# Kernel optimization log

Measured on AMD Instinct MI355X. Metric: run time of the kernel, lower is better.

Reference implementation:

```python
import jax, jax.numpy as jnp
import numpy as np

INPUT_DIM = 1024
OUTPUT_DIM = 1024
DEGREE = 8


def setup_inputs() -> dict:
    key = jax.random.key(0)
    k1, k2 = jax.random.split(key)
    x = jax.random.normal(k1, (8192, INPUT_DIM), dtype=jnp.float32)
    std = 1.0 / (INPUT_DIM * (DEGREE + 1))
    cheby_coeffs = std * jax.random.normal(k2, (INPUT_DIM, OUTPUT_DIM, DEGREE + 1), dtype=jnp.float32)
    return {"x": x, "cheby_coeffs": cheby_coeffs}


def reference(x, cheby_coeffs):
    # x: (B, I); cheby_coeffs: (I, O, D+1)
    degree = cheby_coeffs.shape[-1] - 1
    xt = jnp.tanh(x.reshape(-1, cheby_coeffs.shape[0]))
    # Chebyshev recurrence T_0=1, T_1=x, T_k = 2*x*T_{k-1} - T_{k-2}
    polys = [jnp.ones_like(xt)]
    if degree > 0:
        polys.append(xt)
    for _ in range(2, degree + 1):
        polys.append(2.0 * xt * polys[-1] - polys[-2])
    cheby = jnp.stack(polys, axis=-1)  # (B, I, D+1)
    y = jnp.einsum('bid,iod->bo', cheby, cheby_coeffs)
    return y
```

## Files before the change

### kernel.cpp

```cpp
#include <hip/hip_runtime.h>
#include <hip/hip_bf16.h>

#define AS1 __attribute__((address_space(1)))
#define AS3 __attribute__((address_space(3)))

typedef __attribute__((ext_vector_type(8))) short bf16x8;
typedef __attribute__((ext_vector_type(4))) float f32x4;

#define KTOT 9216
#define NOUT 1024

__device__ __forceinline__ void gll16(const void* g, void* l) {
    __builtin_amdgcn_global_load_lds((const AS1 void*)g, (AS3 void*)l, 16, 0, 0);
}

__device__ __forceinline__ unsigned short f2bf(float f) {
    union { __hip_bfloat16 h; unsigned short u; } cv;
    cv.h = __float2bfloat16(f);
    return cv.u;
}

__device__ __forceinline__ float fast_tanhf(float v) {
    float e = __expf(2.0f * v);
    return 1.0f - 2.0f / (e + 1.0f);
}

__global__ void __launch_bounds__(256) prep_kernel(const float* __restrict__ cc,
                                                   unsigned short* __restrict__ Wt) {
    __shared__ unsigned short T[288 * 68];
    const int t  = threadIdx.x;
    const int n0 = (blockIdx.x & 31) * 32;
    const int i0 = (blockIdx.x >> 5) * 64;

    for (int il = 0; il < 64; ++il) {
        const float* src = cc + (size_t)(i0 + il) * KTOT + (size_t)n0 * 9;
        for (int f = t; f < 288; f += 256)
            T[f * 68 + il] = f2bf(src[f]);
    }
    __syncthreads();

    for (int it = 0; it < 18; ++it) {
        const int chunk = it * 16 + (t >> 4);
        const int nl = chunk / 9;
        const int d  = chunk - nl * 9;
        const int n  = n0 + nl;
        const int e0 = (t & 15) * 4;
        const int isrc = e0 ^ ((n & 7) << 3);
        ushort4 v = *(const ushort4*)&T[chunk * 68 + isrc];
        *(ushort4*)(Wt + (size_t)n * KTOT + d * 1024 + i0 + e0) = v;
    }
}

__global__ void __launch_bounds__(256, 2)
cheby_gemm(const float* __restrict__ x, const unsigned short* __restrict__ Wt,
           float* __restrict__ out) {
    __shared__ unsigned short Asub[128 * 64];
    __shared__ unsigned short Bsub[128 * 64];

    const int id   = blockIdx.x;
    const int bcol = (id & 7) * 128;
    const int brow = (id >> 3) * 128;
    const int t    = threadIdx.x;
    const int lane = t & 63;
    const int w    = t >> 6;
    const int wr   = (w >> 1) * 64;
    const int wc   = (w & 1) * 64;
    const int l15  = lane & 15;
    const int lhi  = lane >> 4;

    const int gi0 = (t & 15) * 4;
    const int gr  = t >> 4;

    const int bn_loc = t >> 3;
    const int bpos   = (t & 7) * 8;

    f32x4 acc[4][4] = {};

    float x2[8][4], Tp[8][4], Tpp[8][4];

    unsigned awoff[8];
#pragma unroll
    for (int p = 0; p < 8; ++p) {
        const int r = gr + 16 * p;
        awoff[p] = r * 128 + ((gi0 * 2) ^ ((r & 7) << 4));
    }

    for (int ic = 0; ic < 16; ++ic) {
#pragma unroll
        for (int p = 0; p < 8; ++p) {
            const float4 v = *(const float4*)(x + (size_t)(brow + gr + 16 * p) * 1024
                                              + ic * 64 + gi0);
            x2[p][0] = 2.0f * fast_tanhf(v.x);
            x2[p][1] = 2.0f * fast_tanhf(v.y);
            x2[p][2] = 2.0f * fast_tanhf(v.z);
            x2[p][3] = 2.0f * fast_tanhf(v.w);
        }
#pragma unroll
        for (int d = 0; d < 9; ++d) {
            __syncthreads();

            const int kb = d * 1024 + ic * 64;
#pragma unroll
            for (int c = 0; c < 4; ++c) {
                const unsigned short* src =
                    Wt + (size_t)(bcol + c * 32 + bn_loc) * KTOT + kb + bpos;
                gll16(src, (char*)Bsub + c * 4096 + w * 1024);
            }

#pragma unroll
            for (int p = 0; p < 8; ++p) {
                ushort4 pk;
                unsigned short* pks = (unsigned short*)&pk;
#pragma unroll
                for (int j = 0; j < 4; ++j) {
                    float cur;
                    if (d == 0) {
                        cur = 1.0f;
                    } else if (d == 1) {
                        cur = 0.5f * x2[p][j];
                        Tp[p][j] = cur;
                        Tpp[p][j] = 1.0f;
                    } else {
                        cur = __builtin_fmaf(x2[p][j], Tp[p][j], -Tpp[p][j]);
                        Tpp[p][j] = Tp[p][j];
                        Tp[p][j] = cur;
                    }
                    pks[j] = f2bf(cur);
                }
                *(ushort4*)((char*)Asub + awoff[p]) = pk;
            }

            __syncthreads();

#pragma unroll
            for (int ks = 0; ks < 2; ++ks) {
                bf16x8 af[4], bfr[4];
#pragma unroll
                for (int mf = 0; mf < 4; ++mf) {
                    const int row = wr + mf * 16 + l15;
                    af[mf] = *(const bf16x8*)((const char*)Asub + row * 128 +
                              ((ks * 64 + lhi * 16) ^ ((row & 7) << 4)));
                }
#pragma unroll
                for (int nf = 0; nf < 4; ++nf) {
                    const int n = wc + nf * 16 + l15;
                    bfr[nf] = *(const bf16x8*)((const char*)Bsub + n * 128 +
                              ((ks * 64 + lhi * 16) ^ ((n & 7) << 4)));
                }
#pragma unroll
                for (int mf = 0; mf < 4; ++mf)
#pragma unroll
                    for (int nf = 0; nf < 4; ++nf)
                        acc[mf][nf] = __builtin_amdgcn_mfma_f32_16x16x32_bf16(
                            af[mf], bfr[nf], acc[mf][nf], 0, 0, 0);
            }
        }
    }

#pragma unroll
    for (int mf = 0; mf < 4; ++mf)
#pragma unroll
        for (int nf = 0; nf < 4; ++nf)
#pragma unroll
            for (int ri = 0; ri < 4; ++ri) {
                const int orow = brow + wr + mf * 16 + lhi * 4 + ri;
                const int ocol = bcol + wc + nf * 16 + l15;
                out[(size_t)orow * NOUT + ocol] = acc[mf][nf][ri];
            }
}

__global__ void __launch_bounds__(256) naive_kernel(const float* __restrict__ x,
                                                    const float* __restrict__ cc,
                                                    float* __restrict__ out) {
    __shared__ float xs[1024];
    const int b = blockIdx.x;
    const int t = threadIdx.x;
#pragma unroll
    for (int j = 0; j < 4; ++j)
        xs[t * 4 + j] = fast_tanhf(x[(size_t)b * 1024 + t * 4 + j]);
    __syncthreads();

    const int o = t * 4;
    float a0 = 0.f, a1 = 0.f, a2 = 0.f, a3 = 0.f;
    for (int i = 0; i < 1024; ++i) {
        const float* cp = cc + (size_t)i * KTOT + (size_t)o * 9;
        const float xv = xs[i];
        float tpp = 1.0f, tp = xv;
        a0 += cp[0];  a1 += cp[9];  a2 += cp[18];  a3 += cp[27];
        a0 += xv * cp[1]; a1 += xv * cp[10]; a2 += xv * cp[19]; a3 += xv * cp[28];
#pragma unroll
        for (int d = 2; d <= 8; ++d) {
            const float cur = 2.0f * xv * tp - tpp;
            tpp = tp; tp = cur;
            a0 += cur * cp[d];      a1 += cur * cp[9 + d];
            a2 += cur * cp[18 + d]; a3 += cur * cp[27 + d];
        }
    }
    float* op = out + (size_t)b * NOUT + o;
    op[0] = a0; op[1] = a1; op[2] = a2; op[3] = a3;
}

extern "C" void kernel_launch(void* const* d_in, const int* in_sizes, int n_in,
                              void* d_out, int out_size, void* d_ws, size_t ws_size,
                              hipStream_t stream) {
    const float* x  = (const float*)d_in[0];
    const float* cc = (const float*)d_in[1];
    float* out = (float*)d_out;

    const size_t need = (size_t)KTOT * 1024 * sizeof(unsigned short);
    if (ws_size >= need) {
        prep_kernel<<<512, 256, 0, stream>>>(cc, (unsigned short*)d_ws);
        cheby_gemm<<<512, 256, 0, stream>>>(x, (const unsigned short*)d_ws, out);
    } else {
        naive_kernel<<<8192, 256, 0, stream>>>(x, cc, out);
    }
}
```

Before: 232.3 us.

## Fold T0 term into bias, load B fragments from global with double-buffered A tile

Removes the degree-0 Chebyshev term from the GEMM: because T0=1, its contribution is a per-output bias (sum of coefficients over inputs), which prep_kernel computes with atomics and the epilogue adds. This shrinks K from 9216 to 8192. The GEMM tile becomes 64x256 with each wave reading B fragments straight from global into registers, prefetched one step ahead. A is double-buffered in LDS so each step needs only one barrier. In exchange it adds a memset and atomics, and direct global B loads may be less coalesced than the previous LDS staging.

Result: slower. 312.7 us (+34.6%).

```diff
diff --git a/kernel.cpp b/kernel.cpp
--- a/kernel.cpp
+++ b/kernel.cpp
@@ -1,171 +1,202 @@
 #include <hip/hip_runtime.h>
 #include <hip/hip_bf16.h>
 
-#define AS1 __attribute__((address_space(1)))
-#define AS3 __attribute__((address_space(3)))
-
 typedef __attribute__((ext_vector_type(8))) short bf16x8;
 typedef __attribute__((ext_vector_type(4))) float f32x4;
 
-#define KTOT 9216
+#define CSTRIDE 9216
+#define KT2 8192
 #define NOUT 1024
 
-__device__ __forceinline__ void gll16(const void* g, void* l) {
-    __builtin_amdgcn_global_load_lds((const AS1 void*)g, (AS3 void*)l, 16, 0, 0);
-}
-
-__device__ __forceinline__ unsigned short f2bf(float f) {
+static __device__ __forceinline__ unsigned short f2bf(float f) {
     union { __hip_bfloat16 h; unsigned short u; } cv;
     cv.h = __float2bfloat16(f);
     return cv.u;
 }
-
-__device__ __forceinline__ float fast_tanhf(float v) {
+static __device__ __forceinline__ float bf2f(unsigned short u) {
+    union { float f; unsigned v; } c; c.v = (unsigned)u << 16; return c.f;
+}
+static __device__ __forceinline__ float fast_tanhf(float v) {
     float e = __expf(2.0f * v);
     return 1.0f - 2.0f / (e + 1.0f);
 }
 
 __global__ void __launch_bounds__(256) prep_kernel(const float* __restrict__ cc,
-                                                   unsigned short* __restrict__ Wt) {
+                                                   unsigned short* __restrict__ Wt,
+                                                   float* __restrict__ bias) {
     __shared__ unsigned short T[288 * 68];
     const int t  = threadIdx.x;
     const int n0 = (blockIdx.x & 31) * 32;
     const int i0 = (blockIdx.x >> 5) * 64;
 
     for (int il = 0; il < 64; ++il) {
-        const float* src = cc + (size_t)(i0 + il) * KTOT + (size_t)n0 * 9;
+        const float* src = cc + (size_t)(i0 + il) * CSTRIDE + (size_t)n0 * 9;
         for (int f = t; f < 288; f += 256)
             T[f * 68 + il] = f2bf(src[f]);
     }
     __syncthreads();
 
-    for (int it = 0; it < 18; ++it) {
+#pragma unroll
+    for (int it = 0; it < 16; ++it) {
         const int chunk = it * 16 + (t >> 4);
-        const int nl = chunk / 9;
-        const int d  = chunk - nl * 9;
-        const int n  = n0 + nl;
+        const int nl = chunk >> 3;
+        const int d  = (chunk & 7) + 1;
         const int e0 = (t & 15) * 4;
-        const int isrc = e0 ^ ((n & 7) << 3);
-        ushort4 v = *(const ushort4*)&T[chunk * 68 + isrc];
-        *(ushort4*)(Wt + (size_t)n * KTOT + d * 1024 + i0 + e0) = v;
+        ushort4 v = *(const ushort4*)&T[(nl * 9 + d) * 68 + e0];
+        *(ushort4*)(Wt + (size_t)(n0 + nl) * KT2 + (d - 1) * 1024 + i0 + e0) = v;
+    }
+
+    if (t < 32) {
+        float s = 0.f;
+#pragma unroll 8
+        for (int il = 0; il < 64; ++il) s += bf2f(T[(t * 9) * 68 + il]);
+        atomicAdd(&bias[n0 + t], s);
     }
 }
 
 __global__ void __launch_bounds__(256, 2)
 cheby_gemm(const float* __restrict__ x, const unsigned short* __restrict__ Wt,
-           float* __restrict__ out) {
-    __shared__ unsigned short Asub[128 * 64];
-    __shared__ unsigned short Bsub[128 * 64];
+           const float* __restrict__ bias, float* __restrict__ out) {
+    __shared__ unsigned short Asub[2][64 * 64];
 
     const int id   = blockIdx.x;
-    const int bcol = (id & 7) * 128;
-    const int brow = (id >> 3) * 128;
+    const int bcol = (id & 3) * 256;
+    const int brow = (id >> 2) * 64;
     const int t    = threadIdx.x;
     const int lane = t & 63;
     const int w    = t >> 6;
-    const int wr   = (w >> 1) * 64;
-    const int wc   = (w & 1) * 64;
+    const int wc   = w * 64;
     const int l15  = lane & 15;
     const int lhi  = lane >> 4;
 
     const int gi0 = (t & 15) * 4;
-    const int gr  = t >> 4;
-
-    const int bn_loc = t >> 3;
-    const int bpos   = (t & 7) * 8;
+    const int rr  = t >> 4;
+
+    unsigned awoff[4];
+#pragma unroll
+    for (int p = 0; p < 4; ++p) {
+        const int r = rr + 16 * p;
+        awoff[p] = r * 128 + ((gi0 * 2) ^ ((r & 7) << 4));
+    }
 
     f32x4 acc[4][4] = {};
-
-    float x2[8][4], Tp[8][4], Tpp[8][4];
-
-    unsigned awoff[8];
-#pragma unroll
-    for (int p = 0; p < 8; ++p) {
-        const int r = gr + 16 * p;
-        awoff[p] = r * 128 + ((gi0 * 2) ^ ((r & 7) << 4));
-    }
-
+    float x2[4][4], Tp[4][4], Tpp[4][4];
+    bf16x8 bcur[2][4];
+
+    const unsigned short* wbase = Wt + (size_t)(bcol + wc) * KT2 + lhi * 8;
+
+#pragma unroll
+    for (int p = 0; p < 4; ++p) {
+        const float4 v = *(const float4*)(x + (size_t)(brow + rr + 16 * p) * 1024 + gi0);
+        ushort4 pk; unsigned short* pks = (unsigned short*)&pk;
+#pragma unroll
+        for (int j = 0; j < 4; ++j) {
+            const float xv = (&v.x)[j];
+            x2[p][j] = 2.0f * fast_tanhf(xv);
+            const float c = 0.5f * x2[p][j];
+            Tp[p][j] = c; Tpp[p][j] = 1.0f;
+            pks[j] = f2bf(c);
+        }
+        *(ushort4*)((char*)Asub[0] + awoff[p]) = pk;
+    }
+#pragma unroll
+    for (int ks = 0; ks < 2; ++ks)
+#pragma unroll
+        for (int nf = 0; nf < 4; ++nf)
+            bcur[ks][nf] = *(const bf16x8*)(wbase + (size_t)(nf * 16 + l15) * KT2 + ks * 32);
+    asm volatile("s_waitcnt lgkmcnt(0)" ::: "memory");
+    __builtin_amdgcn_s_barrier();
+
+#pragma unroll 1
     for (int ic = 0; ic < 16; ++ic) {
 #pragma unroll
-        for (int p = 0; p < 8; ++p) {
-            const float4 v = *(const float4*)(x + (size_t)(brow + gr + 16 * p) * 1024
-                                              + ic * 64 + gi0);
-            x2[p][0] = 2.0f * fast_tanhf(v.x);
-            x2[p][1] = 2.0f * fast_tanhf(v.y);
-            x2[p][2] = 2.0f * fast_tanhf(v.z);
-            x2[p][3] = 2.0f * fast_tanhf(v.w);
-        }
-#pragma unroll
-        for (int d = 0; d < 9; ++d) {
-            __syncthreads();
-
-            const int kb = d * 1024 + ic * 64;
-#pragma unroll
-            for (int c = 0; c < 4; ++c) {
-                const unsigned short* src =
-                    Wt + (size_t)(bcol + c * 32 + bn_loc) * KTOT + kb + bpos;
-                gll16(src, (char*)Bsub + c * 4096 + w * 1024);
+        for (int dd = 0; dd < 8; ++dd) {
+            const int cur = dd & 1;
+            const int nxt = cur ^ 1;
+            const int ddn = (dd + 1) & 7;
+            const int icn = (dd == 7) ? ((ic + 1) & 15) : ic;
+            const int kbn = ddn * 1024 + icn * 64;
+
+            bf16x8 bnxt[2][4];
+#pragma unroll
+            for (int ks = 0; ks < 2; ++ks)
+#pragma unroll
+                for (int nf = 0; nf < 4; ++nf)
+                    bnxt[ks][nf] = *(const bf16x8*)(wbase + (size_t)(nf * 16 + l15) * KT2
+                                                    + kbn + ks * 32);
+
+            bf16x8 af[2][4];
+#pragma unroll
+            for (int ks = 0; ks < 2; ++ks)
+#pragma unroll
+                for (int mf = 0; mf < 4; ++mf) {
+                    const int row = mf * 16 + l15;
+                    af[ks][mf] = *(const bf16x8*)((const char*)Asub[cur] + row * 128 +
+                                  ((ks * 64 + lhi * 16) ^ ((row & 7) << 4)));
+                }
+
+            if (dd == 7) {
+#pragma unroll
+                for (int p = 0; p < 4; ++p) {
+                    const float4 v = *(const float4*)(x + (size_t)(brow + rr + 16 * p) * 1024
+                                                      + icn * 64 + gi0);
+                    ushort4 pk; unsigned short* pks = (unsigned short*)&pk;
+#pragma unroll
+                    for (int j = 0; j < 4; ++j) {
+                        const float xv = (&v.x)[j];
+                        x2[p][j] = 2.0f * fast_tanhf(xv);
+                        const float c = 0.5f * x2[p][j];
+                        Tp[p][j] = c; Tpp[p][j] = 1.0f;
+                        pks[j] = f2bf(c);
+                    }
+                    *(ushort4*)((char*)Asub[nxt] + awoff[p]) = pk;
+                }
+            } else {
+#pragma unroll
+                for (int p = 0; p < 4; ++p) {
+                    ushort4 pk; unsigned short* pks = (unsigned short*)&pk;
+#pragma unroll
+                    for (int j = 0; j < 4; ++j) {
+                        const float c = __builtin_fmaf(x2[p][j], Tp[p][j], -Tpp[p][j]);
+                        Tpp[p][j] = Tp[p][j]; Tp[p][j] = c;
+                        pks[j] = f2bf(c);
+                    }
+                    *(ushort4*)((char*)Asub[nxt] + awoff[p]) = pk;
+                }
             }
 
 #pragma unroll
-            for (int p = 0; p < 8; ++p) {
-                ushort4 pk;
-                unsigned short* pks = (unsigned short*)&pk;
-#pragma unroll
-                for (int j = 0; j < 4; ++j) {
-                    float cur;
-                    if (d == 0) {
-                        cur = 1.0f;
-                    } else if (d == 1) {
-                        cur = 0.5f * x2[p][j];
-                        Tp[p][j] = cur;
-                        Tpp[p][j] = 1.0f;
-                    } else {
-                        cur = __builtin_fmaf(x2[p][j], Tp[p][j], -Tpp[p][j]);
-                        Tpp[p][j] = Tp[p][j];
-                        Tp[p][j] = cur;
-                    }
-                    pks[j] = f2bf(cur);
-                }
-                *(ushort4*)((char*)Asub + awoff[p]) = pk;
-            }
-
-            __syncthreads();
-
-#pragma unroll
-            for (int ks = 0; ks < 2; ++ks) {
-                bf16x8 af[4], bfr[4];
-#pragma unroll
-                for (int mf = 0; mf < 4; ++mf) {
-                    const int row = wr + mf * 16 + l15;
-                    af[mf] = *(const bf16x8*)((const char*)Asub + row * 128 +
-                              ((ks * 64 + lhi * 16) ^ ((row & 7) << 4)));
-                }
-#pragma unroll
-                for (int nf = 0; nf < 4; ++nf) {
-                    const int n = wc + nf * 16 + l15;
-                    bfr[nf] = *(const bf16x8*)((const char*)Bsub + n * 128 +
-                              ((ks * 64 + lhi * 16) ^ ((n & 7) << 4)));
-                }
+            for (int ks = 0; ks < 2; ++ks)
 #pragma unroll
                 for (int mf = 0; mf < 4; ++mf)
 #pragma unroll
                     for (int nf = 0; nf < 4; ++nf)
                         acc[mf][nf] = __builtin_amdgcn_mfma_f32_16x16x32_bf16(
-                            af[mf], bfr[nf], acc[mf][nf], 0, 0, 0);
-            }
+                            af[ks][mf], bcur[ks][nf], acc[mf][nf], 0, 0, 0);
+
+            asm volatile("s_waitcnt lgkmcnt(0)" ::: "memory");
+            __builtin_amdgcn_s_barrier();
+
+#pragma unroll
+            for (int ks = 0; ks < 2; ++ks)
+#pragma unroll
+                for (int nf = 0; nf < 4; ++nf)
+                    bcur[ks][nf] = bnxt[ks][nf];
         }
     }
 
+    float bv[4];
+#pragma unroll
+    for (int nf = 0; nf < 4; ++nf) bv[nf] = bias[bcol + wc + nf * 16 + l15];
 #pragma unroll
     for (int mf = 0; mf < 4; ++mf)
 #pragma unroll
         for (int nf = 0; nf < 4; ++nf)
 #pragma unroll
             for (int ri = 0; ri < 4; ++ri) {
-                const int orow = brow + wr + mf * 16 + lhi * 4 + ri;
+                const int orow = brow + mf * 16 + lhi * 4 + ri;
                 const int ocol = bcol + wc + nf * 16 + l15;
-                out[(size_t)orow * NOUT + ocol] = acc[mf][nf][ri];
+                out[(size_t)orow * NOUT + ocol] = acc[mf][nf][ri] + bv[nf];
             }
 }
 
@@ -183,7 +214,7 @@
     const int o = t * 4;
     float a0 = 0.f, a1 = 0.f, a2 = 0.f, a3 = 0.f;
     for (int i = 0; i < 1024; ++i) {
-        const float* cp = cc + (size_t)i * KTOT + (size_t)o * 9;
+        const float* cp = cc + (size_t)i * CSTRIDE + (size_t)o * 9;
         const float xv = xs[i];
         float tpp = 1.0f, tp = xv;
         a0 += cp[0];  a1 += cp[9];  a2 += cp[18];  a3 += cp[27];
@@ -207,10 +238,14 @@
     const float* cc = (const float*)d_in[1];
     float* out = (float*)d_out;
 
-    const size_t need = (size_t)KTOT * 1024 * sizeof(unsigned short);
+    const size_t wt_bytes = (size_t)KT2 * 1024 * sizeof(unsigned short);
+    const size_t need = wt_bytes + 1024 * sizeof(float);
     if (ws_size >= need) {
-        prep_kernel<<<512, 256, 0, stream>>>(cc, (unsigned short*)d_ws);
-        cheby_gemm<<<512, 256, 0, stream>>>(x, (const unsigned short*)d_ws, out);
+        unsigned short* Wt = (unsigned short*)d_ws;
+        float* bias = (float*)((char*)d_ws + wt_bytes);
+        hipMemsetAsync(bias, 0, 1024 * sizeof(float), stream);
+        prep_kernel<<<512, 256, 0, stream>>>(cc, Wt, bias);
+        cheby_gemm<<<512, 256, 0, stream>>>(x, Wt, bias, out);
     } else {
         naive_kernel<<<8192, 256, 0, stream>>>(x, cc, out);
     }
```
